# Optimization experiments

Hardware: AMD Instinct MI355X
Metric: run time of the kernel (lower is better)

## Reference

```python
import jax, jax.numpy as jnp
import numpy as np

NUM_POINTS = 72
GAMMA = 2.0
RADIUS = 15.0
W_CLS = 1.0
W_SIM = 3.0
LW_CLS = 2.0
LW_XYTL = 0.5
LW_LIOU = 2.0
K_MAX = 64
EPS = 1e-12  # F.normalize eps


def _normalize(v):
    # F.normalize over the flattened prior axis: v / max(||v||_2, eps)
    return v / jnp.maximum(jnp.linalg.norm(v), EPS)


def _liou_loss(pred, tgt):
    # pred: [..., P], tgt broadcastable; line IoU with radius, loss = 1 - iou
    lo = jnp.minimum(pred, tgt)
    hi = jnp.maximum(pred, tgt)
    ovr = (lo + RADIUS) - (hi - RADIUS)          # per-point overlap (may be < 0)
    union = (hi + RADIUS) - (lo - RADIUS)
    iou = jnp.sum(ovr, -1) / (jnp.sum(union, -1) + 1e-9)
    return 1.0 - iou


def _per_lane(feature, prior):
    # feature: [N, D] predictions for one image; prior: [D] one GT lane
    # ---- assignment cost ----
    logits = feature[:, :2]
    log_s = jax.nn.log_softmax(logits, axis=0)   # softmax over the N priors dim (dim=1 of [1,N,2])
    s = jnp.exp(log_s)
    focal_cost = jnp.sum(((1.0 - s) ** GAMMA) * log_s * prior[:2], axis=-1)  # [N]
    xy_cost = _normalize(jnp.sqrt(jnp.sum((feature[:, 3:5] - prior[3:5]) ** 2, -1)))  # [N]
    theta_cost = _normalize(feature[:, 5] - prior[5])                                  # [N]
    dis_cost = _normalize(jnp.sum(jnp.abs(feature[:, 6:] - prior[6:]), -1) / NUM_POINTS)  # [N]
    cost = W_SIM * (dis_cost * xy_cost * theta_cost) ** 2 + W_CLS * focal_cost
    # ---- dynamic top-k ----
    liou_all = _liou_loss(feature[:, 6:], prior[None, 6:])  # [N]
    k = jnp.clip(jnp.sum(liou_all).astype(jnp.int32), 1, K_MAX)
    _, idx = jax.lax.top_k(-cost, K_MAX)  # sorted ascending by cost; first k == topk(-cost, k)
    mask = (jnp.arange(K_MAX) < k).astype(feature.dtype)  # [K]
    kf = jnp.sum(mask)
    pf = feature[idx]  # [K, D] gathered predicted features
    # ---- xytl smooth-L1 on column-normalized concat([pred[:,2:6]; label[2:6]]) over valid rows ----
    rows = pf[:, 2:6]          # [K, 4]
    lab = prior[2:6]           # [4]
    colnorm = jnp.sqrt(jnp.sum((rows ** 2) * mask[:, None], 0) + lab ** 2)  # norm over the k+1 rows
    denom = jnp.maximum(colnorm, EPS)
    d = rows / denom - lab / denom  # [K, 4]
    ad = jnp.abs(d)
    sl1 = jnp.mean(jnp.where(ad < 1.0, 0.5 * d * d, ad - 0.5), -1)  # [K]
    sl1l = jnp.sum(sl1 * mask) / kf
    # ---- focal cls loss per assigned prior vs argmax of label cls ----
    tgt = jnp.argmax(prior[:2])
    lp = jax.nn.log_softmax(pf[:, :2], axis=-1)  # [K, 2]
    logpt = lp[:, tgt]
    pt = jnp.exp(logpt)
    fl_i = -((1.0 - pt) ** GAMMA) * logpt  # [K]
    fl = jnp.sum(fl_i * mask) / kf
    # ---- LIoU loss on assigned priors ----
    ll_i = _liou_loss(pf[:, 6:], prior[None, 6:])  # [K]
    ll = jnp.sum(ll_i * mask) / kf
    return sl1l, ll, fl


def setup_inputs() -> dict:
    key = jax.random.key(0)
    k1, k2 = jax.random.split(key)
    output = jax.random.normal(k1, (64, 1000, 78), dtype=jnp.float32)
    label = jax.random.normal(k2, (64, 16, 78), dtype=jnp.float32)
    return {"output": output, "label": label}


def reference(output, label):
    per_img = jax.vmap(_per_lane, in_axes=(None, 0))        # over lanes
    sl1l, ll, fl = jax.vmap(per_img, in_axes=(0, 0))(output, label)  # over batch
    sl1l = jnp.mean(sl1l)
    ll = jnp.mean(ll)
    fl = jnp.mean(fl)
    loss = (jnp.where(sl1l > 0, LW_XYTL * sl1l, 0.0)
            + jnp.where(ll > 0, LW_LIOU * ll, 0.0)
            + jnp.where(fl > 0, LW_CLS * fl, 0.0))
    return loss
```

## Files before the change

### kernel.cpp

```cpp
#include <hip/hip_runtime.h>
#include <math.h>

#define NROWS 1000
#define TWO_R_N 2160.0f
typedef unsigned int uint;
typedef unsigned long long ull;

__device__ __forceinline__ float wsumf(float v){
#pragma unroll
  for(int o=32;o;o>>=1) v += __shfl_xor(v,o,64);
  return v;
}
__device__ __forceinline__ float wmaxf(float v){
#pragma unroll
  for(int o=32;o;o>>=1) v = fmaxf(v,__shfl_xor(v,o,64));
  return v;
}

__device__ __forceinline__ void dma16(const float4* g, float4* l){
  __builtin_amdgcn_global_load_lds((const __attribute__((address_space(1))) void*)g,
                                   (__attribute__((address_space(3))) void*)l,
                                   16, 0, 0);
}

__global__ __launch_bounds__(256,4) void clr_task(const float* __restrict__ feat,
                                                  const float* __restrict__ lab,
                                                  float* __restrict__ ws)
{
  const int b = blockIdx.x & 63;
  const int l = blockIdx.x >> 6;
  const float* __restrict__ F = feat + (size_t)b*NROWS*78;
  const float* __restrict__ P = lab + ((size_t)b*16 + l)*78;

  __shared__ __align__(16) float4 sBuf4[1280];
  __shared__ float sS[NROWS];
  __shared__ float sRT[NROWS];
  __shared__ float sC0[NROWS];
  __shared__ float sC1[NROWS];
  __shared__ float red[16];
  __shared__ int selIdx[64];

  const int tid=threadIdx.x, wave=tid>>6, lane=tid&63;
  const int rloc = tid>>2, q = tid&3;

  float pv[18];
#pragma unroll
  for(int s=0;s<18;++s) pv[s] = P[6+q+4*s];
  const float2* Pf2 = (const float2*)P;
  const float2 p01=Pf2[0], p23=Pf2[1], p45=Pf2[2];

  float accR=0.f, accT=0.f, accD=0.f, accL=0.f;

  for(int c=0;c<16;++c){
    __syncthreads();
    {
      const float4* src4=(const float4*)(F + (size_t)c*4992);
      const int limit = (c==15)?779:1247;
#pragma unroll
      for(int it=0;it<5;++it){
        int base = it*256 + wave*64;
        int idx  = base + lane;
        dma16(src4 + (idx>limit?limit:idx), sBuf4 + base);
      }
    }
    __syncthreads();
    const int rows = (c<15)?64:40;
    if(rloc<rows){
      const float* rp = (const float*)sBuf4 + rloc*78;
      float part=0.f;
#pragma unroll
      for(int s=0;s<9;++s){
        part += fabsf(rp[6+q+4*s]      - pv[s]);
        part += fabsf(rp[6+q+4*(s+9)]  - pv[s+9]);
      }
      float s1 = part + __shfl_xor(part,1,64);
      float S  = s1   + __shfl_xor(s1,  2,64);
      if(q==0){
        int r = c*64 + rloc;
        const float2* rp2=(const float2*)rp;
        float2 c01=rp2[0], c23=rp2[1], c45=rp2[2];
        float dr3=c23.y-p23.y, dr4=c45.x-p45.x;
        float r2=dr3*dr3+dr4*dr4;
        float tt=c45.y-p45.y;
        sS[r]=S; sRT[r]=sqrtf(r2)*tt; sC0[r]=c01.x; sC1[r]=c01.y;
        accR+=r2; accT+=tt*tt;
        float dd=S*(1.f/72.f); accD+=dd*dd;
        accL += 1.f-(TWO_R_N-S)/(TWO_R_N+S+1e-9f);
      }
    }
  }

  {
    float vR=wsumf(accR), vT=wsumf(accT), vD=wsumf(accD), vL=wsumf(accL);
    if(lane==0){ red[wave*4]=vR; red[wave*4+1]=vT; red[wave*4+2]=vD; red[wave*4+3]=vL; }
  }
  __syncthreads();
  if (wave != 0) return;

  float R=0.f,T=0.f,D=0.f,L=0.f;
#pragma unroll
  for(int w=0;w<4;w++){ R+=red[w*4]; T+=red[w*4+1]; D+=red[w*4+2]; L+=red[w*4+3]; }
  float Nr=fmaxf(sqrtf(R),1e-12f), Nt=fmaxf(sqrtf(T),1e-12f), Nd=fmaxf(sqrtf(D),1e-12f);
  const float inv = 1.f/(Nr*Nt*Nd);
  int k=(int)L; if(k<1)k=1; if(k>64)k=64;

  float m0=-INFINITY, m1=-INFINITY;
#pragma unroll
  for(int t=0;t<16;++t){ int i=t*64+lane; if(i<NROWS){ m0=fmaxf(m0,sC0[i]); m1=fmaxf(m1,sC1[i]);} }
  m0=wmaxf(m0); m1=wmaxf(m1);
  float s0=0.f, s1=0.f;
#pragma unroll
  for(int t=0;t<16;++t){ int i=t*64+lane; if(i<NROWS){ s0+=__expf(sC0[i]-m0); s1+=__expf(sC1[i]-m1);} }
  s0=wsumf(s0); s1=wsumf(s1);
  const float lse0=m0+__logf(s0), lse1=m1+__logf(s1);

  uint key[16];
  const float p0=p01.x, pp1=p01.y;
#pragma unroll
  for(int t=0;t<16;++t){
    int i=t*64+lane; uint kk=0xFFFFFFFFu;
    if(i<NROWS){
      float ls0=sC0[i]-lse0, ls1=sC1[i]-lse1;
      float e0=__expf(ls0), e1=__expf(ls1);
      float focal=(1.f-e0)*(1.f-e0)*ls0*p0 + (1.f-e1)*(1.f-e1)*ls1*pp1;
      float prod=sRT[i]*(sS[i]*(1.f/72.f))*inv;
      float cost=3.f*prod*prod+focal;
      uint x=__float_as_uint(cost);
      kk=(x&0x80000000u)?~x:(x|0x80000000u);
    }
    key[t]=kk;
  }

  uint pref=0u, r=(uint)k;
  for(int s=31;s>=0;--s){
    const uint pp=pref>>s;
    uint cnt=0u;
#pragma unroll
    for(int t=0;t<16;++t) cnt += (uint)__popcll(__ballot((key[t]>>s)==pp));
    if(r>cnt){ r-=cnt; pref|=(1u<<s); }
  }
  const uint T2=pref; uint need=r;

  const ull lmask=(1ull<<lane)-1ull;
  int base=0;
#pragma unroll
  for(int t=0;t<16;++t){
    bool lt = key[t]<T2;
    bool eq = key[t]==T2;
    ull meq=__ballot(eq);
    bool eqs = eq && ((uint)__popcll(meq&lmask)<need);
    uint teq=(uint)__popcll(meq);
    need -= (teq<need?teq:need);
    bool ssel = lt||eqs;
    ull ms=__ballot(ssel);
    if(ssel) selIdx[base+(int)__popcll(ms&lmask)] = t*64+lane;
    base += (int)__popcll(ms);
  }

  {
    bool act = lane<k;
    int idx = selIdx[act?lane:0];
    const float2* R2=(const float2*)(F+(size_t)idx*78);
    float2 g01=R2[0], g23=R2[1], g45=R2[2];
    float S = sS[idx];
    float mk = act?1.f:0.f;
    float n2=wsumf(g23.x*g23.x*mk), n3=wsumf(g23.y*g23.y*mk);
    float n4=wsumf(g45.x*g45.x*mk), n5=wsumf(g45.y*g45.y*mk);
    float l2=p23.x, l3=p23.y, l4=p45.x, l5=p45.y;
    float de2=fmaxf(sqrtf(n2+l2*l2),1e-12f);
    float de3=fmaxf(sqrtf(n3+l3*l3),1e-12f);
    float de4=fmaxf(sqrtf(n4+l4*l4),1e-12f);
    float de5=fmaxf(sqrtf(n5+l5*l5),1e-12f);
    float d2=g23.x/de2-l2/de2, d3=g23.y/de3-l3/de3, d4=g45.x/de4-l4/de4, d5=g45.y/de5-l5/de5;
    auto h=[](float d){ float ad=fabsf(d); return ad<1.f ? 0.5f*d*d : ad-0.5f; };
    float sl1 = 0.25f*(h(d2)+h(d3)+h(d4)+h(d5));
    float mm=fmaxf(g01.x,g01.y);
    float lsee=mm+__logf(__expf(g01.x-mm)+__expf(g01.y-mm));
    float logpt=((pp1>p0)?g01.y:g01.x)-lsee;
    float pt=__expf(logpt);
    float fl=-(1.f-pt)*(1.f-pt)*logpt;
    float ll=1.f-(TWO_R_N-S)/(TWO_R_N+S+1e-9f);
    float ssl=wsumf(sl1*mk), sll=wsumf(ll*mk), sfl=wsumf(fl*mk);
    if(lane==0){
      float invk=1.f/(float)k;
      float* o = ws + (size_t)(b*16+l)*3;
      o[0]=ssl*invk; o[1]=sll*invk; o[2]=sfl*invk;
    }
  }
}

__global__ __launch_bounds__(256) void clr_finalize(const float* __restrict__ ws,
                                                    float* __restrict__ out)
{
  float a=0.f, bsum=0.f, c=0.f;
  for(int i=threadIdx.x;i<1024;i+=256){
    a    += ws[i*3+0];
    bsum += ws[i*3+1];
    c    += ws[i*3+2];
  }
  a=wsumf(a); bsum=wsumf(bsum); c=wsumf(c);
  __shared__ float r[12];
  int wave=threadIdx.x>>6, lane=threadIdx.x&63;
  if(lane==0){ r[wave*3]=a; r[wave*3+1]=bsum; r[wave*3+2]=c; }
  __syncthreads();
  if(threadIdx.x==0){
    float sa=0,sb=0,sc=0;
    for(int w=0;w<4;w++){sa+=r[w*3];sb+=r[w*3+1];sc+=r[w*3+2];}
    float sl1l=sa*(1.f/1024.f), ll=sb*(1.f/1024.f), fl=sc*(1.f/1024.f);
    float loss = (sl1l>0.f ? 0.5f*sl1l : 0.f)
               + (ll  >0.f ? 2.0f*ll   : 0.f)
               + (fl  >0.f ? 2.0f*fl   : 0.f);
    out[0]=loss;
  }
}

extern "C" void kernel_launch(void* const* d_in, const int* in_sizes, int n_in,
                              void* d_out, int out_size, void* d_ws, size_t ws_size,
                              hipStream_t stream)
{
  const float* feat = (const float*)d_in[0];
  const float* lab  = (const float*)d_in[1];
  float* ws  = (float*)d_ws;
  float* out = (float*)d_out;
  hipLaunchKernelGGL(clr_task, dim3(1024), dim3(256), 0, stream, feat, lab, ws);
  hipLaunchKernelGGL(clr_finalize, dim3(1), dim3(256), 0, stream, ws, out);
}
```

Before: 101.2 us.

## Process four lanes per block with shared feature tiles and double-buffered DMA

Each block now handles four GT lanes of one image using 1024 threads, so each 64-row feature chunk is loaded into LDS once and reused by four lanes instead of being reloaded per lane. The LDS chunk loads are double-buffered so the next chunk's DMA is issued while the current chunk is processed, removing one barrier per iteration. Per-lane selection then runs on four waves in parallel. The cost is a much larger LDS footprint, one block per CU, and fewer blocks in flight (256 instead of 1024), which can hurt latency hiding.

```diff
diff --git a/kernel.cpp b/kernel.cpp
--- a/kernel.cpp
+++ b/kernel.cpp
@@ -23,26 +23,27 @@
                                    16, 0, 0);
 }
 
-__global__ __launch_bounds__(256,4) void clr_task(const float* __restrict__ feat,
-                                                  const float* __restrict__ lab,
-                                                  float* __restrict__ ws)
+__global__ __launch_bounds__(1024,1) void clr_task(const float* __restrict__ feat,
+                                                   const float* __restrict__ lab,
+                                                   float* __restrict__ ws)
 {
-  const int b = blockIdx.x & 63;
-  const int l = blockIdx.x >> 6;
+  const int b  = blockIdx.x & 63;
+  const int pg = blockIdx.x >> 6;
   const float* __restrict__ F = feat + (size_t)b*NROWS*78;
-  const float* __restrict__ P = lab + ((size_t)b*16 + l)*78;
-
-  __shared__ __align__(16) float4 sBuf4[1280];
-  __shared__ float sS[NROWS];
-  __shared__ float sRT[NROWS];
-  __shared__ float sC0[NROWS];
-  __shared__ float sC1[NROWS];
-  __shared__ float red[16];
-  __shared__ int selIdx[64];
+
+  __shared__ __align__(16) float4 sBuf4[2][1280];
+  __shared__ float sS[4][NROWS];
+  __shared__ float sRT[4][NROWS];
+  __shared__ float sC0[NROWS], sC1[NROWS];
+  __shared__ float red[64];
+  __shared__ int selIdx[4][64];
 
   const int tid=threadIdx.x, wave=tid>>6, lane=tid&63;
-  const int rloc = tid>>2, q = tid&3;
-
+  const int pw = wave & 3;
+  const int rg = wave >> 2;
+  const int rloc16 = lane>>2, q = lane&3;
+
+  const float* __restrict__ P = lab + ((size_t)b*16 + pg*4 + pw)*78;
   float pv[18];
 #pragma unroll
   for(int s=0;s<18;++s) pv[s] = P[6+q+4*s];
@@ -51,38 +52,53 @@
 
   float accR=0.f, accT=0.f, accD=0.f, accL=0.f;
 
+  {
+    const float4* src4=(const float4*)F;
+#pragma unroll
+    for(int it=0;it<2;++it){
+      int base = it*1024 + wave*64;
+      if(base<=1247){
+        int idx = base + lane;
+        dma16(src4 + (idx>1247?1247:idx), &sBuf4[0][base]);
+      }
+    }
+  }
+
   for(int c=0;c<16;++c){
     __syncthreads();
-    {
-      const float4* src4=(const float4*)(F + (size_t)c*4992);
-      const int limit = (c==15)?779:1247;
-#pragma unroll
-      for(int it=0;it<5;++it){
-        int base = it*256 + wave*64;
-        int idx  = base + lane;
-        dma16(src4 + (idx>limit?limit:idx), sBuf4 + base);
-      }
-    }
-    __syncthreads();
+    if(c<15){
+      const int limit = (c+1==15)?779:1247;
+      const float4* src4=(const float4*)(F + (size_t)(c+1)*4992);
+#pragma unroll
+      for(int it=0;it<2;++it){
+        int base = it*1024 + wave*64;
+        if(base<=limit){
+          int idx = base + lane;
+          dma16(src4 + (idx>limit?limit:idx), &sBuf4[(c+1)&1][base]);
+        }
+      }
+    }
     const int rows = (c<15)?64:40;
-    if(rloc<rows){
-      const float* rp = (const float*)sBuf4 + rloc*78;
+    const int rr = rg*16 + rloc16;
+    if(rr<rows){
+      const float* rp = (const float*)(&sBuf4[c&1][0]) + rr*78;
       float part=0.f;
 #pragma unroll
       for(int s=0;s<9;++s){
-        part += fabsf(rp[6+q+4*s]      - pv[s]);
-        part += fabsf(rp[6+q+4*(s+9)]  - pv[s+9]);
+        part += fabsf(rp[6+q+4*s]     - pv[s]);
+        part += fabsf(rp[6+q+4*(s+9)] - pv[s+9]);
       }
       float s1 = part + __shfl_xor(part,1,64);
       float S  = s1   + __shfl_xor(s1,  2,64);
       if(q==0){
-        int r = c*64 + rloc;
+        int r = c*64 + rr;
         const float2* rp2=(const float2*)rp;
         float2 c01=rp2[0], c23=rp2[1], c45=rp2[2];
         float dr3=c23.y-p23.y, dr4=c45.x-p45.x;
         float r2=dr3*dr3+dr4*dr4;
         float tt=c45.y-p45.y;
-        sS[r]=S; sRT[r]=sqrtf(r2)*tt; sC0[r]=c01.x; sC1[r]=c01.y;
+        sS[pw][r]=S; sRT[pw][r]=sqrtf(r2)*tt;
+        if(pw==0){ sC0[r]=c01.x; sC1[r]=c01.y; }
         accR+=r2; accT+=tt*tt;
         float dd=S*(1.f/72.f); accD+=dd*dd;
         accL += 1.f-(TWO_R_N-S)/(TWO_R_N+S+1e-9f);
@@ -95,11 +111,15 @@
     if(lane==0){ red[wave*4]=vR; red[wave*4+1]=vT; red[wave*4+2]=vD; red[wave*4+3]=vL; }
   }
   __syncthreads();
-  if (wave != 0) return;
+  if (wave >= 4) return;
+  const int w = wave;
 
   float R=0.f,T=0.f,D=0.f,L=0.f;
 #pragma unroll
-  for(int w=0;w<4;w++){ R+=red[w*4]; T+=red[w*4+1]; D+=red[w*4+2]; L+=red[w*4+3]; }
+  for(int g=0;g<4;++g){
+    int src=(4*g+w)*4;
+    R+=red[src]; T+=red[src+1]; D+=red[src+2]; L+=red[src+3];
+  }
   float Nr=fmaxf(sqrtf(R),1e-12f), Nt=fmaxf(sqrtf(T),1e-12f), Nd=fmaxf(sqrtf(D),1e-12f);
   const float inv = 1.f/(Nr*Nt*Nd);
   int k=(int)L; if(k<1)k=1; if(k>64)k=64;
@@ -123,7 +143,7 @@
       float ls0=sC0[i]-lse0, ls1=sC1[i]-lse1;
       float e0=__expf(ls0), e1=__expf(ls1);
       float focal=(1.f-e0)*(1.f-e0)*ls0*p0 + (1.f-e1)*(1.f-e1)*ls1*pp1;
-      float prod=sRT[i]*(sS[i]*(1.f/72.f))*inv;
+      float prod=sRT[w][i]*(sS[w][i]*(1.f/72.f))*inv;
       float cost=3.f*prod*prod+focal;
       uint x=__float_as_uint(cost);
       kk=(x&0x80000000u)?~x:(x|0x80000000u);
@@ -153,16 +173,16 @@
     need -= (teq<need?teq:need);
     bool ssel = lt||eqs;
     ull ms=__ballot(ssel);
-    if(ssel) selIdx[base+(int)__popcll(ms&lmask)] = t*64+lane;
+    if(ssel) selIdx[w][base+(int)__popcll(ms&lmask)] = t*64+lane;
     base += (int)__popcll(ms);
   }
 
   {
     bool act = lane<k;
-    int idx = selIdx[act?lane:0];
+    int idx = selIdx[w][act?lane:0];
     const float2* R2=(const float2*)(F+(size_t)idx*78);
     float2 g01=R2[0], g23=R2[1], g45=R2[2];
-    float S = sS[idx];
+    float S = sS[w][idx];
     float mk = act?1.f:0.f;
     float n2=wsumf(g23.x*g23.x*mk), n3=wsumf(g23.y*g23.y*mk);
     float n4=wsumf(g45.x*g45.x*mk), n5=wsumf(g45.y*g45.y*mk);
@@ -183,7 +203,7 @@
     float ssl=wsumf(sl1*mk), sll=wsumf(ll*mk), sfl=wsumf(fl*mk);
     if(lane==0){
       float invk=1.f/(float)k;
-      float* o = ws + (size_t)(b*16+l)*3;
+      float* o = ws + (size_t)(b*16 + pg*4 + w)*3;
       o[0]=ssl*invk; o[1]=sll*invk; o[2]=sfl*invk;
     }
   }
@@ -205,7 +225,7 @@
   __syncthreads();
   if(threadIdx.x==0){
     float sa=0,sb=0,sc=0;
-    for(int w=0;w<4;w++){sa+=r[w*3];sb+=r[w*3+1];sc+=r[w*3+2];}
+    for(int w2=0;w2<4;w2++){sa+=r[w2*3];sb+=r[w2*3+1];sc+=r[w2*3+2];}
     float sl1l=sa*(1.f/1024.f), ll=sb*(1.f/1024.f), fl=sc*(1.f/1024.f);
     float loss = (sl1l>0.f ? 0.5f*sl1l : 0.f)
                + (ll  >0.f ? 2.0f*ll   : 0.f)
@@ -222,6 +242,6 @@
   const float* lab  = (const float*)d_in[1];
   float* ws  = (float*)d_ws;
   float* out = (float*)d_out;
-  hipLaunchKernelGGL(clr_task, dim3(1024), dim3(256), 0, stream, feat, lab, ws);
+  hipLaunchKernelGGL(clr_task, dim3(256), dim3(1024), 0, stream, feat, lab, ws);
   hipLaunchKernelGGL(clr_finalize, dim3(1), dim3(256), 0, stream, ws, out);
 }
```

Result: no change. 100.4 us (-0.8%).
